# Performance work log

Hardware: AMD Instinct MI355X
Metric: run time of the kernel (lower is better)

## Reference

```python
import jax, jax.numpy as jnp
import numpy as np

BITS = 2
GROUP_SIZE = 128
EPS = 1e-8


def fake_quant(w):
    """Per-group (contiguous 128-element, over flattened weight) min/max fake quantization."""
    max_q = (1 << BITS) - 1  # 3 for INT2
    flat = w.reshape(-1, GROUP_SIZE)            # [num_groups, group_size]
    mn = flat.min(axis=1, keepdims=True)
    mx = flat.max(axis=1, keepdims=True)
    rng = mx - mn
    scale = rng / max_q
    safe_scale = jnp.where(rng < EPS, 1.0, scale)  # avoid div-by-zero
    q = jnp.clip(jnp.round((flat - mn) / safe_scale), 0, max_q)
    deq = q * scale + mn
    out = jnp.where(rng < EPS, flat, deq)        # pass-through for near-constant groups
    return out.reshape(w.shape)


def setup_inputs() -> dict:
    key = jax.random.key(0)
    kx, kw, kb = jax.random.split(key, 3)
    B, S, D_IN, D_OUT = 4, 2048, 4096, 4096
    x = jax.random.normal(kx, (B, S, D_IN), dtype=jnp.float32)
    # kaiming-uniform-like init scale
    bound = float(np.sqrt(6.0 / D_IN))
    weight = jax.random.uniform(kw, (D_OUT, D_IN), minval=-bound, maxval=bound, dtype=jnp.float32)
    bias = jnp.zeros((D_OUT,), dtype=jnp.float32)
    return {"x": x, "weight": weight, "bias": bias}


def reference(x, weight, bias):
    # training-mode forward: STE fake-quant of weight, then linear
    w_quant = weight + jax.lax.stop_gradient(fake_quant(weight) - weight)
    return jnp.einsum('bsd,od->bso', x, w_quant) + bias
```

## Files before the change

kernel.cpp:

```cpp
#include <hip/hip_runtime.h>
#include <hip/hip_bf16.h>
#include <stdint.h>

#define M_DIM 8192
#define N_DIM 4096
#define K_DIM 4096

typedef __hip_bfloat16 bf16;
typedef __attribute__((ext_vector_type(8))) short bf16x8;
typedef __attribute__((ext_vector_type(4))) float floatx4;

__device__ __forceinline__ uint2 pack_bf16x4(float4 v) {
  bf16 b0 = __float2bfloat16(v.x);
  bf16 b1 = __float2bfloat16(v.y);
  bf16 b2 = __float2bfloat16(v.z);
  bf16 b3 = __float2bfloat16(v.w);
  unsigned int lo = (unsigned int)*(unsigned short*)&b0 |
                    ((unsigned int)*(unsigned short*)&b1 << 16);
  unsigned int hi = (unsigned int)*(unsigned short*)&b2 |
                    ((unsigned int)*(unsigned short*)&b3 << 16);
  return make_uint2(lo, hi);
}

__global__ void quant_w_kernel(const float* __restrict__ w, bf16* __restrict__ wq) {
  const int t = blockIdx.x * blockDim.x + threadIdx.x;
  const int g = t >> 4;
  const int s = t & 15;

  const float4* p = (const float4*)(w + (size_t)g * 128);
  float4 a = p[s];
  float4 b = p[s + 16];

  float mn = fminf(fminf(fminf(a.x, a.y), fminf(a.z, a.w)),
                   fminf(fminf(b.x, b.y), fminf(b.z, b.w)));
  float mx = fmaxf(fmaxf(fmaxf(a.x, a.y), fmaxf(a.z, a.w)),
                   fmaxf(fmaxf(b.x, b.y), fmaxf(b.z, b.w)));
#pragma unroll
  for (int off = 8; off >= 1; off >>= 1) {
    mn = fminf(mn, __shfl_xor(mn, off));
    mx = fmaxf(mx, __shfl_xor(mx, off));
  }
  const float rng = mx - mn;
  float4 oa, ob;
  if (rng < 1e-8f) {
    oa = a; ob = b;
  } else {
    const float scale = rng / 3.0f;
    float q0 = fminf(fmaxf(rintf((a.x - mn) / scale), 0.f), 3.f);
    float q1 = fminf(fmaxf(rintf((a.y - mn) / scale), 0.f), 3.f);
    float q2 = fminf(fmaxf(rintf((a.z - mn) / scale), 0.f), 3.f);
    float q3 = fminf(fmaxf(rintf((a.w - mn) / scale), 0.f), 3.f);
    float q4 = fminf(fmaxf(rintf((b.x - mn) / scale), 0.f), 3.f);
    float q5 = fminf(fmaxf(rintf((b.y - mn) / scale), 0.f), 3.f);
    float q6 = fminf(fmaxf(rintf((b.z - mn) / scale), 0.f), 3.f);
    float q7 = fminf(fmaxf(rintf((b.w - mn) / scale), 0.f), 3.f);
    oa = make_float4(q0 * scale + mn, q1 * scale + mn, q2 * scale + mn, q3 * scale + mn);
    ob = make_float4(q4 * scale + mn, q5 * scale + mn, q6 * scale + mn, q7 * scale + mn);
  }
  uint2* q = (uint2*)(wq + (size_t)g * 128);
  q[s]      = pack_bf16x4(oa);
  q[s + 16] = pack_bf16x4(ob);
}

__global__ void cast_x_kernel(const float* __restrict__ x, bf16* __restrict__ xb) {
  const size_t base = (size_t)blockIdx.x * 512;
  const int tid = threadIdx.x;
  const float4* p = (const float4*)x + base;
  float4 a = p[tid];
  float4 b = p[tid + 256];
  uint2* q = (uint2*)xb + base;
  q[tid]       = pack_bf16x4(a);
  q[tid + 256] = pack_bf16x4(b);
}

#define BM 128
#define BN 128
#define BK 64

typedef const uint32_t GQ __attribute__((address_space(1)));
typedef uint32_t LQ __attribute__((address_space(3)));

__global__ void gemm_bt_kernel(const bf16* __restrict__ A,
                               const bf16* __restrict__ Bw,
                               const float* __restrict__ bias,
                               float* __restrict__ C) {
  __shared__ bf16 sA[BM * BK];
  __shared__ bf16 sB[BN * BK];

  const int tid  = threadIdx.x;
  const int lane = tid & 63;
  const int warp = tid >> 6;
  const int wm   = warp & 1;
  const int wn   = warp >> 1;
  const int m0   = blockIdx.y * BM;
  const int n0   = blockIdx.x * BN;

  floatx4 acc[4][4];
#pragma unroll
  for (int i = 0; i < 4; ++i)
#pragma unroll
    for (int j = 0; j < 4; ++j)
      acc[i][j] = (floatx4){0.f, 0.f, 0.f, 0.f};

  const int srow   = warp * 8 + (lane >> 3);
  const int schunk = (lane & 7) ^ ((lane >> 3) & 7);
  const int scol   = schunk * 8;

  const int fr  = lane & 15;
  const int fs  = lane & 7;
  const int fc  = lane >> 4;

  for (int k0 = 0; k0 < K_DIM; k0 += BK) {
#pragma unroll
    for (int j = 0; j < 4; ++j) {
      const int r = j * 32 + srow;
      const bf16* g = A + (size_t)(m0 + r) * K_DIM + (k0 + scol);
      bf16* l = sA + (j * 32 + warp * 8) * BK;
      __builtin_amdgcn_global_load_lds((GQ*)g, (LQ*)l, 16, 0, 0);
    }
#pragma unroll
    for (int j = 0; j < 4; ++j) {
      const int r = j * 32 + srow;
      const bf16* g = Bw + (size_t)(n0 + r) * K_DIM + (k0 + scol);
      bf16* l = sB + (j * 32 + warp * 8) * BK;
      __builtin_amdgcn_global_load_lds((GQ*)g, (LQ*)l, 16, 0, 0);
    }
    __syncthreads();

#pragma unroll
    for (int kk = 0; kk < BK; kk += 32) {
      const int chnk = (((kk >> 3) + fc) ^ fs) * 8;
      bf16x8 af[4], bfr[4];
#pragma unroll
      for (int i = 0; i < 4; ++i)
        af[i] = *(const bf16x8*)&sA[(wm * 64 + i * 16 + fr) * BK + chnk];
#pragma unroll
      for (int j = 0; j < 4; ++j)
        bfr[j] = *(const bf16x8*)&sB[(wn * 64 + j * 16 + fr) * BK + chnk];
#pragma unroll
      for (int i = 0; i < 4; ++i)
#pragma unroll
        for (int j = 0; j < 4; ++j)
          acc[i][j] = __builtin_amdgcn_mfma_f32_16x16x32_bf16(af[i], bfr[j], acc[i][j], 0, 0, 0);
    }
    __syncthreads();
  }

  const int cm = (lane >> 4) * 4;
  const int cn = lane & 15;
#pragma unroll
  for (int j = 0; j < 4; ++j) {
    const int col = n0 + wn * 64 + j * 16 + cn;
    const float bv = bias[col];
#pragma unroll
    for (int i = 0; i < 4; ++i) {
      const int rowb = m0 + wm * 64 + i * 16 + cm;
      float* out = C + (size_t)rowb * N_DIM + col;
#pragma unroll
      for (int r = 0; r < 4; ++r)
        out[(size_t)r * N_DIM] = acc[i][j][r] + bv;
    }
  }
}

extern "C" void kernel_launch(void* const* d_in, const int* in_sizes, int n_in,
                              void* d_out, int out_size, void* d_ws, size_t ws_size,
                              hipStream_t stream) {
  const float* x      = (const float*)d_in[0];
  const float* weight = (const float*)d_in[1];
  const float* bias   = (const float*)d_in[2];
  float* out          = (float*)d_out;

  bf16* wq = (bf16*)d_ws;
  bf16* xb = (bf16*)((char*)d_ws + (size_t)N_DIM * K_DIM * sizeof(bf16));

  {
    int threads = (N_DIM * K_DIM) / 8;
    quant_w_kernel<<<threads / 256, 256, 0, stream>>>(weight, wq);
  }
  {
    int threads = (M_DIM * K_DIM) / 8;
    cast_x_kernel<<<threads / 256, 256, 0, stream>>>(x, xb);
  }
  {
    dim3 grid(N_DIM / BN, M_DIM / BM);
    gemm_bt_kernel<<<grid, 256, 0, stream>>>(xb, wq, bias, out);
  }
}
```

Measured before the change: 509.1 us.

## Enlarge GEMM tile to 256x256 with double-buffered LDS and phased MFMA schedule

Replaces the 128x128 single-buffered GEMM with a 256x256 tile run by 512 threads. Global-to-LDS loads are double-buffered so the next K tile is fetched while the current one is computed. Each K tile is split into four phases of LDS reads and MFMA blocks, separated by barriers and priority hints. The larger tile increases operand reuse and the pipelining hides load latency, at the cost of 128 KB of dynamic LDS, many more accumulator registers and a grid of only 512 blocks.

```diff
diff --git a/kernel.cpp b/kernel.cpp
--- a/kernel.cpp
+++ b/kernel.cpp
@@ -9,6 +9,9 @@
 typedef __hip_bfloat16 bf16;
 typedef __attribute__((ext_vector_type(8))) short bf16x8;
 typedef __attribute__((ext_vector_type(4))) float floatx4;
+
+typedef const uint32_t GQ __attribute__((address_space(1)));
+typedef uint32_t LQ __attribute__((address_space(3)));
 
 __device__ __forceinline__ uint2 pack_bf16x4(float4 v) {
   bf16 b0 = __float2bfloat16(v.x);
@@ -73,77 +76,187 @@
   q[tid + 256] = pack_bf16x4(b);
 }
 
-#define BM 128
-#define BN 128
+#define BM 256
+#define BN 256
 #define BK 64
-
-typedef const uint32_t GQ __attribute__((address_space(1)));
-typedef uint32_t LQ __attribute__((address_space(3)));
-
-__global__ void gemm_bt_kernel(const bf16* __restrict__ A,
-                               const bf16* __restrict__ Bw,
-                               const float* __restrict__ bias,
-                               float* __restrict__ C) {
-  __shared__ bf16 sA[BM * BK];
-  __shared__ bf16 sB[BN * BK];
+#define NT (K_DIM / BK)
+
+#define MFMA_BF16 __builtin_amdgcn_mfma_f32_16x16x32_bf16
+
+__device__ __forceinline__ bf16x8 lds_read_b128(const bf16* p) {
+  bf16x8 r;
+  asm volatile("ds_read_b128 %0, %1" : "=v"(r) : "v"((const LQ*)p));
+  return r;
+}
+
+__device__ __forceinline__ void stage_tile(const bf16* __restrict__ Ag,
+                                           const bf16* __restrict__ Bg,
+                                           bf16* sa, bf16* sb,
+                                           int k0, int warp, int lane) {
+  const int srow = warp * 8 + (lane >> 3);
+  const int scol = ((lane & 7) ^ ((lane >> 3) & 7)) * 8;
+#pragma unroll
+  for (int j = 0; j < 4; ++j) {
+    const bf16* g = Ag + (size_t)(j * 64 + srow) * K_DIM + (k0 + scol);
+    bf16* l = sa + (j * 64 + warp * 8) * BK;
+    __builtin_amdgcn_global_load_lds((GQ*)g, (LQ*)l, 16, 0, 0);
+  }
+#pragma unroll
+  for (int j = 0; j < 4; ++j) {
+    const bf16* g = Bg + (size_t)(j * 64 + srow) * K_DIM + (k0 + scol);
+    bf16* l = sb + (j * 64 + warp * 8) * BK;
+    __builtin_amdgcn_global_load_lds((GQ*)g, (LQ*)l, 16, 0, 0);
+  }
+}
+
+#define PHASE_WAIT()                                    \
+  __builtin_amdgcn_s_barrier();                         \
+  __builtin_amdgcn_sched_barrier(0);                    \
+  asm volatile("s_waitcnt lgkmcnt(0)" ::: "memory");    \
+  __builtin_amdgcn_sched_barrier(0);                    \
+  __builtin_amdgcn_s_setprio(1)
+
+#define PHASE_CLOSE()                                   \
+  __builtin_amdgcn_s_setprio(0);                        \
+  __builtin_amdgcn_sched_barrier(0);                    \
+  __builtin_amdgcn_s_barrier();                         \
+  __builtin_amdgcn_sched_barrier(0)
+
+__device__ __forceinline__ void do_ktile(const bf16* sa, const bf16* sb,
+                                         floatx4 (&acc)[8][4],
+                                         const int aBase, const int bBase,
+                                         const int c0, const int c1) {
+  bf16x8 af[4][2];
+  bf16x8 bfr[2][2];
+
+#pragma unroll
+  for (int i = 0; i < 4; ++i) {
+    af[i][0] = lds_read_b128(sa + aBase + i * 16 * BK + c0);
+    af[i][1] = lds_read_b128(sa + aBase + i * 16 * BK + c1);
+  }
+#pragma unroll
+  for (int j = 0; j < 2; ++j) {
+    bfr[j][0] = lds_read_b128(sb + bBase + j * 16 * BK + c0);
+    bfr[j][1] = lds_read_b128(sb + bBase + j * 16 * BK + c1);
+  }
+  PHASE_WAIT();
+#pragma unroll
+  for (int s = 0; s < 2; ++s)
+#pragma unroll
+    for (int i = 0; i < 4; ++i)
+#pragma unroll
+      for (int j = 0; j < 2; ++j)
+        acc[i][j] = MFMA_BF16(af[i][s], bfr[j][s], acc[i][j], 0, 0, 0);
+  PHASE_CLOSE();
+
+#pragma unroll
+  for (int j = 0; j < 2; ++j) {
+    bfr[j][0] = lds_read_b128(sb + bBase + (2 + j) * 16 * BK + c0);
+    bfr[j][1] = lds_read_b128(sb + bBase + (2 + j) * 16 * BK + c1);
+  }
+  PHASE_WAIT();
+#pragma unroll
+  for (int s = 0; s < 2; ++s)
+#pragma unroll
+    for (int i = 0; i < 4; ++i)
+#pragma unroll
+      for (int j = 0; j < 2; ++j)
+        acc[i][2 + j] = MFMA_BF16(af[i][s], bfr[j][s], acc[i][2 + j], 0, 0, 0);
+  PHASE_CLOSE();
+
+#pragma unroll
+  for (int i = 0; i < 4; ++i) {
+    af[i][0] = lds_read_b128(sa + aBase + (4 + i) * 16 * BK + c0);
+    af[i][1] = lds_read_b128(sa + aBase + (4 + i) * 16 * BK + c1);
+  }
+  PHASE_WAIT();
+#pragma unroll
+  for (int s = 0; s < 2; ++s)
+#pragma unroll
+    for (int i = 0; i < 4; ++i)
+#pragma unroll
+      for (int j = 0; j < 2; ++j)
+        acc[4 + i][2 + j] = MFMA_BF16(af[i][s], bfr[j][s], acc[4 + i][2 + j], 0, 0, 0);
+  PHASE_CLOSE();
+
+#pragma unroll
+  for (int j = 0; j < 2; ++j) {
+    bfr[j][0] = lds_read_b128(sb + bBase + j * 16 * BK + c0);
+    bfr[j][1] = lds_read_b128(sb + bBase + j * 16 * BK + c1);
+  }
+  PHASE_WAIT();
+#pragma unroll
+  for (int s = 0; s < 2; ++s)
+#pragma unroll
+    for (int i = 0; i < 4; ++i)
+#pragma unroll
+      for (int j = 0; j < 2; ++j)
+        acc[4 + i][j] = MFMA_BF16(af[i][s], bfr[j][s], acc[4 + i][j], 0, 0, 0);
+  PHASE_CLOSE();
+}
+
+__global__ __launch_bounds__(512, 2)
+void gemm_bt_kernel(const bf16* __restrict__ A,
+                    const bf16* __restrict__ Bw,
+                    const float* __restrict__ bias,
+                    float* __restrict__ C) {
+  extern __shared__ bf16 smem[];
+  bf16* sA0 = smem;
+  bf16* sB0 = smem + 1 * BM * BK;
+  bf16* sA1 = smem + 2 * BM * BK;
+  bf16* sB1 = smem + 3 * BM * BK;
 
   const int tid  = threadIdx.x;
   const int lane = tid & 63;
   const int warp = tid >> 6;
-  const int wm   = warp & 1;
-  const int wn   = warp >> 1;
+  const int wm   = warp >> 2;
+  const int wn   = warp & 3;
   const int m0   = blockIdx.y * BM;
   const int n0   = blockIdx.x * BN;
 
-  floatx4 acc[4][4];
-#pragma unroll
-  for (int i = 0; i < 4; ++i)
+  const bf16* Ag = A  + (size_t)m0 * K_DIM;
+  const bf16* Bg = Bw + (size_t)n0 * K_DIM;
+
+  floatx4 acc[8][4];
+#pragma unroll
+  for (int i = 0; i < 8; ++i)
 #pragma unroll
     for (int j = 0; j < 4; ++j)
       acc[i][j] = (floatx4){0.f, 0.f, 0.f, 0.f};
 
-  const int srow   = warp * 8 + (lane >> 3);
-  const int schunk = (lane & 7) ^ ((lane >> 3) & 7);
-  const int scol   = schunk * 8;
-
-  const int fr  = lane & 15;
-  const int fs  = lane & 7;
-  const int fc  = lane >> 4;
-
-  for (int k0 = 0; k0 < K_DIM; k0 += BK) {
-#pragma unroll
-    for (int j = 0; j < 4; ++j) {
-      const int r = j * 32 + srow;
-      const bf16* g = A + (size_t)(m0 + r) * K_DIM + (k0 + scol);
-      bf16* l = sA + (j * 32 + warp * 8) * BK;
-      __builtin_amdgcn_global_load_lds((GQ*)g, (LQ*)l, 16, 0, 0);
+  const int fr = lane & 15;
+  const int fs = lane & 7;
+  const int fc = lane >> 4;
+  const int c0 = ((0 + fc) ^ fs) * 8;
+  const int c1 = ((4 + fc) ^ fs) * 8;
+  const int aBase = (wm * 128 + fr) * BK;
+  const int bBase = (wn * 64 + fr) * BK;
+
+  stage_tile(Ag, Bg, sA0, sB0, 0 * BK, warp, lane);
+  stage_tile(Ag, Bg, sA1, sB1, 1 * BK, warp, lane);
+  asm volatile("s_waitcnt vmcnt(8)" ::: "memory");
+  __builtin_amdgcn_s_barrier();
+  __builtin_amdgcn_sched_barrier(0);
+
+#pragma unroll 1
+  for (int tt = 0; tt < NT; tt += 2) {
+    do_ktile(sA0, sB0, acc, aBase, bBase, c0, c1);
+    if (tt + 2 < NT) {
+      stage_tile(Ag, Bg, sA0, sB0, (tt + 2) * BK, warp, lane);
+      asm volatile("s_waitcnt vmcnt(8)" ::: "memory");
+    } else {
+      asm volatile("s_waitcnt vmcnt(0)" ::: "memory");
     }
-#pragma unroll
-    for (int j = 0; j < 4; ++j) {
-      const int r = j * 32 + srow;
-      const bf16* g = Bw + (size_t)(n0 + r) * K_DIM + (k0 + scol);
-      bf16* l = sB + (j * 32 + warp * 8) * BK;
-      __builtin_amdgcn_global_load_lds((GQ*)g, (LQ*)l, 16, 0, 0);
+    __builtin_amdgcn_s_barrier();
+    __builtin_amdgcn_sched_barrier(0);
+
+    do_ktile(sA1, sB1, acc, aBase, bBase, c0, c1);
+    if (tt + 3 < NT) {
+      stage_tile(Ag, Bg, sA1, sB1, (tt + 3) * BK, warp, lane);
+      asm volatile("s_waitcnt vmcnt(8)" ::: "memory");
+      __builtin_amdgcn_s_barrier();
+      __builtin_amdgcn_sched_barrier(0);
     }
-    __syncthreads();
-
-#pragma unroll
-    for (int kk = 0; kk < BK; kk += 32) {
-      const int chnk = (((kk >> 3) + fc) ^ fs) * 8;
-      bf16x8 af[4], bfr[4];
-#pragma unroll
-      for (int i = 0; i < 4; ++i)
-        af[i] = *(const bf16x8*)&sA[(wm * 64 + i * 16 + fr) * BK + chnk];
-#pragma unroll
-      for (int j = 0; j < 4; ++j)
-        bfr[j] = *(const bf16x8*)&sB[(wn * 64 + j * 16 + fr) * BK + chnk];
-#pragma unroll
-      for (int i = 0; i < 4; ++i)
-#pragma unroll
-        for (int j = 0; j < 4; ++j)
-          acc[i][j] = __builtin_amdgcn_mfma_f32_16x16x32_bf16(af[i], bfr[j], acc[i][j], 0, 0, 0);
-    }
-    __syncthreads();
   }
 
   const int cm = (lane >> 4) * 4;
@@ -153,12 +266,12 @@
     const int col = n0 + wn * 64 + j * 16 + cn;
     const float bv = bias[col];
 #pragma unroll
-    for (int i = 0; i < 4; ++i) {
-      const int rowb = m0 + wm * 64 + i * 16 + cm;
-      float* out = C + (size_t)rowb * N_DIM + col;
+    for (int i = 0; i < 8; ++i) {
+      const int rowb = m0 + wm * 128 + i * 16 + cm;
+      float* outp = C + (size_t)rowb * N_DIM + col;
 #pragma unroll
       for (int r = 0; r < 4; ++r)
-        out[(size_t)r * N_DIM] = acc[i][j][r] + bv;
+        outp[(size_t)r * N_DIM] = acc[i][j][r] + bv;
     }
   }
 }
@@ -183,7 +296,15 @@
     cast_x_kernel<<<threads / 256, 256, 0, stream>>>(x, xb);
   }
   {
+    constexpr int smem_bytes = 4 * BM * BK * (int)sizeof(bf16);
+    static bool attr_done = false;
+    if (!attr_done) {
+      (void)hipFuncSetAttribute((const void*)gemm_bt_kernel,
+                                hipFuncAttributeMaxDynamicSharedMemorySize,
+                                smem_bytes);
+      attr_done = true;
+    }
     dim3 grid(N_DIM / BN, M_DIM / BM);
-    gemm_bt_kernel<<<grid, 256, 0, stream>>>(xb, wq, bias, out);
-  }
-}
+    gemm_bt_kernel<<<grid, 512, smem_bytes, stream>>>(xb, wq, bias, out);
+  }
+}
```

Measured after the change: 520.4 us. 1.02x slower.
